# Optimization experiments

Measured on AMD Instinct MI355X. Metric: run time of the kernel, lower is better.

Reference implementation:

```python
import jax, jax.numpy as jnp
import numpy as np

TEMPERATURE = 0.07
EPS = 1e-8

def setup_inputs() -> dict:
    key = jax.random.key(0)
    k1, k2 = jax.random.split(key)
    features = jax.random.normal(k1, (8192, 512), dtype=jnp.float32)
    labels = jax.random.randint(k2, (8192,), 0, 100, dtype=jnp.int64)
    return {"features": features, "labels": labels}

def reference(features, labels):
    # L2-normalize rows (torch F.normalize uses eps=1e-12 clamp on norm)
    norm = jnp.maximum(jnp.linalg.norm(features, axis=1, keepdims=True), 1e-12)
    f = features / norm                                   # [B, D]
    sim = jnp.matmul(f, f.T) / TEMPERATURE                # [B, B]
    B = features.shape[0]
    same_label = (labels[:, None] == labels[None, :]).astype(features.dtype)
    diag = jnp.eye(B, dtype=bool)
    mask = jnp.where(diag, 0.0, same_label)               # positives, diag removed
    exp_sim = jnp.where(diag, 0.0, jnp.exp(sim))          # diag zeroed
    positive_sum = jnp.sum(exp_sim * mask, axis=1)        # [B]
    negative_sum = jnp.sum(exp_sim * (1.0 - mask), axis=1)
    loss = -jnp.log(positive_sum / (positive_sum + negative_sum + EPS))
    return loss.mean()
```

## Files before the change

### kernel.cpp

```cpp
#include <hip/hip_runtime.h>

#define BATCH 8192
#define DIM   512
#define NBLK  2080

typedef __attribute__((ext_vector_type(2))) long long2_t;
typedef __attribute__((ext_vector_type(4))) float f32x4;
typedef unsigned char u8;

__device__ __forceinline__ void gload_lds16(const void* g, void* l){
  __builtin_amdgcn_global_load_lds(
      (const __attribute__((address_space(1))) void*)g,
      (__attribute__((address_space(3))) void*)l, 16, 0, 0);
}

template<int CTRL>
__device__ __forceinline__ float dpp_add(float v){
  int s = __builtin_amdgcn_update_dpp(0, __float_as_int(v), CTRL, 0xF, 0xF, true);
  return v + __int_as_float(s);
}
__device__ __forceinline__ float red16(float v){
  v = dpp_add<0xB1>(v);
  v = dpp_add<0x4E>(v);
  v = dpp_add<0x141>(v);
  v = dpp_add<0x140>(v);
  return v;
}

__device__ __forceinline__ u8 f2e4m3(float v){
  unsigned s = (__float_as_uint(v) >> 24) & 0x80u;
  float a = fabsf(v);
  if (a < 0.0009765625f) return (u8)s;
  if (a < 0.015625f){
    int qd = (int)rintf(a * 512.0f);
    return (u8)(s | (unsigned)qd);
  }
  unsigned u = __float_as_uint(a);
  int E = (int)(u >> 23) - 127;
  unsigned m = u & 0x7FFFFF;
  unsigned mant = m >> 20;
  unsigned rem  = m & 0xFFFFF;
  mant += (rem > 0x80000u || (rem == 0x80000u && (mant & 1u))) ? 1u : 0u;
  if (mant == 8u){ mant = 0u; E += 1; }
  return (u8)(s | ((unsigned)(E + 7) << 3) | mant);
}

__global__ __launch_bounds__(256) void k_normalize(const float* __restrict__ x,
                                                   u8* __restrict__ q){
  const int row  = blockIdx.x * 4 + (threadIdx.x >> 6);
  const int lane = threadIdx.x & 63;
  const float* xr = x + (size_t)row * DIM + lane * 8;
  float4 a = *(const float4*)xr;
  float4 b = *(const float4*)(xr + 4);
  float s = a.x*a.x + a.y*a.y + a.z*a.z + a.w*a.w
          + b.x*b.x + b.y*b.y + b.z*b.z + b.w*b.w;
  #pragma unroll
  for (int m = 1; m < 64; m <<= 1) s += __shfl_xor(s, m);
  const float inv = 1.0f / fmaxf(sqrtf(s), 1e-12f);
  float f[8] = {a.x, a.y, a.z, a.w, b.x, b.y, b.z, b.w};
  union { u8 b[8]; unsigned long long u; } pk;
  #pragma unroll
  for (int e = 0; e < 8; e++) pk.b[e] = f2e4m3(f[e] * inv);
  const int kb = lane >> 3;
  const int g  = lane & 7;
  const int sw = (row >> 1) & 3;
  const size_t off = (size_t)row * DIM + kb * 64
                   + (size_t)(((g & 3) ^ sw) * 16 + (g >> 2) * 8);
  *(unsigned long long*)(q + off) = pk.u;
}

__global__ __launch_bounds__(256, 3) void k_gemm(const u8* __restrict__ q,
                                                 const int* __restrict__ labels,
                                                 float* __restrict__ ppos,
                                                 float* __restrict__ ptot){
  __shared__ u8 sA[3][128 * 64];
  __shared__ u8 sB[3][128 * 64];
  __shared__ int labI[128], labJ[128];

  const int bid = (blockIdx.x & 7) * 260 + (blockIdx.x >> 3);
  int bj = (int)((sqrtf(8.0f * (float)bid + 1.0f) - 1.0f) * 0.5f);
  while ((bj + 1) * (bj + 2) / 2 <= bid) bj++;
  while (bj * (bj + 1) / 2 > bid) bj--;
  const int bi = bid - bj * (bj + 1) / 2;
  const bool mirror = (bi != bj);
  const int rowbase = bi * 128, colbase = bj * 128;

  const int t    = threadIdx.x;
  const int lane = t & 63;
  const int w    = t >> 6;
  const int wr   = w >> 1, wc = w & 1;
  const int lrow = lane & 15;
  const int g    = lane >> 4;

  if (t < 128) labI[t] = labels[rowbase + t];
  else         labJ[t - 128] = labels[colbase + (t - 128)];

  const int gs = (g ^ ((lrow >> 1) & 3)) * 16;
  int ra[4], rb[4];
  #pragma unroll
  for (int m = 0; m < 4; m++) ra[m] = (wr * 64 + m * 16 + lrow) * 64 + gs;
  #pragma unroll
  for (int n = 0; n < 4; n++) rb[n] = (wc * 64 + n * 16 + lrow) * 64 + gs;

  const u8* srcA = q + (size_t)(rowbase + (t >> 2)) * DIM + (t & 3) * 16;
  const u8* srcB = q + (size_t)(colbase + (t >> 2)) * DIM + (t & 3) * 16;
  const int dL = t * 16;

#define STAGE(BUF, KT) do{                                                \
    gload_lds16(srcA + (KT) * 64,             sA[BUF] + dL);              \
    gload_lds16(srcA + (KT) * 64 + 64 * DIM,  sA[BUF] + dL + 4096);       \
    gload_lds16(srcB + (KT) * 64,             sB[BUF] + dL);              \
    gload_lds16(srcB + (KT) * 64 + 64 * DIM,  sB[BUF] + dL + 4096);       \
  }while(0)

  f32x4 acc[4][4];
  #pragma unroll
  for (int m = 0; m < 4; m++)
    #pragma unroll
    for (int n = 0; n < 4; n++)
      acc[m][n] = (f32x4){0.f, 0.f, 0.f, 0.f};

  STAGE(0, 0);
  STAGE(1, 1);
  __syncthreads();

  #pragma unroll
  for (int kt = 0; kt < 8; ++kt){
    const int cur = kt % 3;
    if (kt < 6) STAGE((kt + 2) % 3, kt + 2);
    const u8* pA = sA[cur];
    const u8* pB = sB[cur];
    long2_t av[4], bv[4];
    #pragma unroll
    for (int n = 0; n < 4; n++) bv[n] = *(const long2_t*)(pB + rb[n]);
    #pragma unroll
    for (int m = 0; m < 4; m++) av[m] = *(const long2_t*)(pA + ra[m]);
    __builtin_amdgcn_s_setprio(1);
    #pragma unroll
    for (int m = 0; m < 4; m++)
      #pragma unroll
      for (int n = 0; n < 4; n++)
        acc[m][n] = __builtin_amdgcn_mfma_f32_16x16x32_fp8_fp8(
            av[m][0], bv[n][0], acc[m][n], 0, 0, 0);
    #pragma unroll
    for (int m = 0; m < 4; m++)
      #pragma unroll
      for (int n = 0; n < 4; n++)
        acc[m][n] = __builtin_amdgcn_mfma_f32_16x16x32_fp8_fp8(
            av[m][1], bv[n][1], acc[m][n], 0, 0, 0);
    __builtin_amdgcn_s_setprio(0);
    if (kt < 6)       asm volatile("s_waitcnt vmcnt(4)" ::: "memory");
    else if (kt == 6) asm volatile("s_waitcnt vmcnt(0)" ::: "memory");
    if (kt < 7) __builtin_amdgcn_s_barrier();
  }
#undef STAGE

  const int i0 = rowbase + wr * 64;
  const int j0 = colbase + wc * 64;

  int lj_[4];
  #pragma unroll
  for (int n = 0; n < 4; n++)
    lj_[n] = labJ[wc * 64 + n * 16 + lrow];

  const float invT = 14.285714285714286f;
  #pragma unroll
  for (int m = 0; m < 4; m++)
    #pragma unroll
    for (int n = 0; n < 4; n++)
      #pragma unroll
      for (int e = 0; e < 4; e++){
        int i = i0 + m * 16 + g * 4 + e;
        int j = j0 + n * 16 + lrow;
        acc[m][n][e] = (i == j) ? 0.0f : __expf(acc[m][n][e] * invT);
      }

  {
    float* pp = ppos + (size_t)(2 * bj + wc) * BATCH;
    float* pt = ptot + (size_t)(2 * bj + wc) * BATCH;
    #pragma unroll
    for (int m = 0; m < 4; m++){
      int li4[4];
      #pragma unroll
      for (int e = 0; e < 4; e++) li4[e] = labI[wr * 64 + m * 16 + g * 4 + e];
      float tr[4] = {0, 0, 0, 0}, pr[4] = {0, 0, 0, 0};
      #pragma unroll
      for (int n = 0; n < 4; n++){
        int lj = lj_[n];
        #pragma unroll
        for (int e = 0; e < 4; e++){
          float v = acc[m][n][e];
          tr[e] += v;
          pr[e] += (li4[e] == lj) ? v : 0.0f;
        }
      }
      #pragma unroll
      for (int e = 0; e < 4; e++){
        tr[e] = red16(tr[e]);
        pr[e] = red16(pr[e]);
      }
      if (lrow == 0){
        int ib = i0 + m * 16 + g * 4;
        #pragma unroll
        for (int e = 0; e < 4; e++){
          pt[ib + e] = tr[e];
          pp[ib + e] = pr[e];
        }
      }
    }
  }

  if (mirror){
    float* pp = ppos + (size_t)(2 * bi + wr) * BATCH;
    float* pt = ptot + (size_t)(2 * bi + wr) * BATCH;
    #pragma unroll
    for (int n = 0; n < 4; n++){
      float ts = 0.f, ps = 0.f;
      int lj = lj_[n];
      #pragma unroll
      for (int m = 0; m < 4; m++){
        int li4[4];
        #pragma unroll
        for (int e = 0; e < 4; e++) li4[e] = labI[wr * 64 + m * 16 + g * 4 + e];
        #pragma unroll
        for (int e = 0; e < 4; e++){
          float v = acc[m][n][e];
          ts += v;
          ps += (li4[e] == lj) ? v : 0.0f;
        }
      }
      ts += __shfl_xor(ts, 16); ps += __shfl_xor(ps, 16);
      ts += __shfl_xor(ts, 32); ps += __shfl_xor(ps, 32);
      if (lane < 16){
        int j = j0 + n * 16 + lane;
        pt[j] = ts;
        pp[j] = ps;
      }
    }
  }
}

__global__ __launch_bounds__(256) void k_rowloss(const float* __restrict__ ppos,
                                                 const float* __restrict__ ptot,
                                                 float* __restrict__ bsum){
  __shared__ float sp[256], st2[256];
  const int t = threadIdx.x;
  const int r = blockIdx.x * 32 + (t & 31);
  const int c0 = t >> 5;
  float p = 0.f, tt = 0.f;
  for (int c = c0; c < 128; c += 8){
    p  += ppos[(size_t)c * BATCH + r];
    tt += ptot[(size_t)c * BATCH + r];
  }
  sp[t] = p; st2[t] = tt;
  __syncthreads();
  if (t < 32){
    float P = 0.f, T = 0.f;
    #pragma unroll
    for (int k = 0; k < 8; k++){ P += sp[t + k * 32]; T += st2[t + k * 32]; }
    sp[t] = -logf(P / (T + 1e-8f));
  }
  __syncthreads();
  if (t == 0){
    float s = 0.f;
    #pragma unroll
    for (int k = 0; k < 32; k++) s += sp[k];
    bsum[blockIdx.x] = s;
  }
}

__global__ __launch_bounds__(256) void k_final(const float* __restrict__ bsum,
                                               float* __restrict__ out){
  __shared__ float s4[4];
  float v = bsum[threadIdx.x];
  #pragma unroll
  for (int m = 1; m < 64; m <<= 1) v += __shfl_xor(v, m);
  if ((threadIdx.x & 63) == 0) s4[threadIdx.x >> 6] = v;
  __syncthreads();
  if (threadIdx.x == 0) out[0] = (s4[0] + s4[1] + s4[2] + s4[3]) * (1.0f / 8192.0f);
}

extern "C" void kernel_launch(void* const* d_in, const int* in_sizes, int n_in,
                              void* d_out, int out_size, void* d_ws, size_t ws_size,
                              hipStream_t stream){
  const float* x      = (const float*)d_in[0];
  const int*   labels = (const int*)d_in[1];
  float*       out    = (float*)d_out;

  char* ws = (char*)d_ws;
  u8*    q    = (u8*)ws;
  float* ppos = (float*)(ws + 8388608);
  float* ptot = (float*)(ws + 8388608 + 4194304);
  float* bsum = (float*)(ws + 8388608 + 8388608);

  k_normalize<<<BATCH / 4, 256, 0, stream>>>(x, q);
  k_gemm<<<NBLK, 256, 0, stream>>>(q, labels, ppos, ptot);
  k_rowloss<<<256, 256, 0, stream>>>(ppos, ptot, bsum);
  k_final<<<1, 256, 0, stream>>>(bsum, out);
}
```

Measured before the change: 56.43 us.

## Use 16x16x128 scaled FP8 MFMA over two K-tiles per iteration

Replaces the 16x16x32 FP8 MFMA with the MI355X scaled f8f6f4 16x16x128 instruction, which consumes two 64-byte K stages per call. The quantized layout swizzle and the LDS read addressing change so each lane gathers 32 bytes across two buffers. The triple-buffer pipeline now loads two stages per iteration and uses full __syncthreads instead of vmcnt-counted barriers. The aim is to cut MFMA issue count and loop overhead, at the cost of less load/compute overlap and more barrier stalls.

```diff
diff --git a/kernel.cpp b/kernel.cpp
--- a/kernel.cpp
+++ b/kernel.cpp
@@ -4,7 +4,8 @@
 #define DIM   512
 #define NBLK  2080
 
-typedef __attribute__((ext_vector_type(2))) long long2_t;
+typedef __attribute__((ext_vector_type(4))) int   int4v;
+typedef __attribute__((ext_vector_type(8))) int   int8v;
 typedef __attribute__((ext_vector_type(4))) float f32x4;
 typedef unsigned char u8;
 
@@ -65,7 +66,7 @@
   const int g  = lane & 7;
   const int sw = (row >> 1) & 3;
   const size_t off = (size_t)row * DIM + kb * 64
-                   + (size_t)(((g & 3) ^ sw) * 16 + (g >> 2) * 8);
+                   + (size_t)(((g >> 1) ^ sw) * 16 + (g & 1) * 8);
   *(unsigned long long*)(q + off) = pk.u;
 }
 
@@ -91,16 +92,18 @@
   const int wr   = w >> 1, wc = w & 1;
   const int lrow = lane & 15;
   const int g    = lane >> 4;
+  const int bufsel = g >> 1;
 
   if (t < 128) labI[t] = labels[rowbase + t];
   else         labJ[t - 128] = labels[colbase + (t - 128)];
 
-  const int gs = (g ^ ((lrow >> 1) & 3)) * 16;
+  const int sw = (lrow >> 1) & 3;
+  const int ph = (((g & 1) * 2) ^ sw) * 16;
   int ra[4], rb[4];
   #pragma unroll
-  for (int m = 0; m < 4; m++) ra[m] = (wr * 64 + m * 16 + lrow) * 64 + gs;
-  #pragma unroll
-  for (int n = 0; n < 4; n++) rb[n] = (wc * 64 + n * 16 + lrow) * 64 + gs;
+  for (int m = 0; m < 4; m++) ra[m] = (wr * 64 + m * 16 + lrow) * 64 + ph;
+  #pragma unroll
+  for (int n = 0; n < 4; n++) rb[n] = (wc * 64 + n * 16 + lrow) * 64 + ph;
 
   const u8* srcA = q + (size_t)(rowbase + (t >> 2)) * DIM + (t & 3) * 16;
   const u8* srcB = q + (size_t)(colbase + (t >> 2)) * DIM + (t & 3) * 16;
@@ -125,33 +128,37 @@
   __syncthreads();
 
   #pragma unroll
-  for (int kt = 0; kt < 8; ++kt){
-    const int cur = kt % 3;
-    if (kt < 6) STAGE((kt + 2) % 3, kt + 2);
-    const u8* pA = sA[cur];
-    const u8* pB = sB[cur];
-    long2_t av[4], bv[4];
-    #pragma unroll
-    for (int n = 0; n < 4; n++) bv[n] = *(const long2_t*)(pB + rb[n]);
-    #pragma unroll
-    for (int m = 0; m < 4; m++) av[m] = *(const long2_t*)(pA + ra[m]);
+  for (int u = 0; u < 4; ++u){
+    const int b_lo = (2 * u) % 3;
+    const int b_hi = (2 * u + 1) % 3;
+    const int b_nx = (2 * u + 2) % 3;
+    const u8* pA = bufsel ? sA[b_hi] : sA[b_lo];
+    const u8* pB = bufsel ? sB[b_hi] : sB[b_lo];
+
+    int8v av[4], bv[4];
+    #pragma unroll
+    for (int n = 0; n < 4; n++){
+      int4v lo = *(const int4v*)(pB + rb[n]);
+      int4v hi = *(const int4v*)(pB + (rb[n] ^ 16));
+      bv[n] = __builtin_shufflevector(lo, hi, 0, 1, 2, 3, 4, 5, 6, 7);
+    }
+    #pragma unroll
+    for (int m = 0; m < 4; m++){
+      int4v lo = *(const int4v*)(pA + ra[m]);
+      int4v hi = *(const int4v*)(pA + (ra[m] ^ 16));
+      av[m] = __builtin_shufflevector(lo, hi, 0, 1, 2, 3, 4, 5, 6, 7);
+    }
+    __syncthreads();
+    if (u < 3){ STAGE(b_nx, 2 * u + 2); STAGE(b_lo, 2 * u + 3); }
     __builtin_amdgcn_s_setprio(1);
     #pragma unroll
     for (int m = 0; m < 4; m++)
       #pragma unroll
       for (int n = 0; n < 4; n++)
-        acc[m][n] = __builtin_amdgcn_mfma_f32_16x16x32_fp8_fp8(
-            av[m][0], bv[n][0], acc[m][n], 0, 0, 0);
-    #pragma unroll
-    for (int m = 0; m < 4; m++)
-      #pragma unroll
-      for (int n = 0; n < 4; n++)
-        acc[m][n] = __builtin_amdgcn_mfma_f32_16x16x32_fp8_fp8(
-            av[m][1], bv[n][1], acc[m][n], 0, 0, 0);
+        acc[m][n] = __builtin_amdgcn_mfma_scale_f32_16x16x128_f8f6f4(
+            av[m], bv[n], acc[m][n], 0, 0, 0, 127, 0, 127);
     __builtin_amdgcn_s_setprio(0);
-    if (kt < 6)       asm volatile("s_waitcnt vmcnt(4)" ::: "memory");
-    else if (kt == 6) asm volatile("s_waitcnt vmcnt(0)" ::: "memory");
-    if (kt < 7) __builtin_amdgcn_s_barrier();
+    __syncthreads();
   }
 #undef STAGE
 
```

Result: slower. 66.22 us (+17.3%).
